# Performance work log

Hardware: AMD Instinct MI355X
Metric: run time of the kernel (lower is better)

## Reference

```python
import jax, jax.numpy as jnp
import numpy as np

B, L, D = 8, 30, 512
NS, NI = 21, 8  # n_slot_caps = n_slots+1, n_intent_caps = n_intents+1


def setup_inputs() -> dict:
    key = jax.random.key(0)
    ks = jax.random.split(key, 6)
    s = 0.02  # keep pose magnitudes sane
    return {
        "token_features": jax.random.normal(ks[0], (B, L, D), jnp.float32),
        "cls_token": jax.random.normal(ks[1], (B, D), jnp.float32),
        "w_route_ws": jax.random.normal(ks[2], (L, NS, D), jnp.float32) * s,
        "w_pose_ws": jax.random.normal(ks[3], (L, NS, D, D), jnp.float32) * s,
        "w_route_si": jax.random.normal(ks[4], (NS, NI, D), jnp.float32) * s,
        "w_pose_si": jax.random.normal(ks[5], (NS, NI, D, D), jnp.float32) * s,
    }


def reference(token_features, cls_token, w_route_ws, w_pose_ws, w_route_si, w_pose_si):
    d_model = token_features.shape[-1]
    # ---- route words -> slots ----
    a_words = token_features.sum(-1) / d_model                      # (b, l)
    c_ws = jax.nn.softmax(
        jnp.einsum('lnj,blj->bln', w_route_ws, token_features), axis=-1)  # (b, l, n_slot)
    wc = c_ws * a_words[:, :, None]                                 # (b, l, n_slot)
    weighted_c = wc.sum(axis=1)                                     # (b, n_slot)
    a_slots = weighted_c / a_words.sum(-1, keepdims=True)           # (b, n_slot)
    u_hat_slots = jnp.einsum('lnij,blj->blni', w_pose_ws, token_features)  # (b, l, n_slot, d)
    u_slots = jnp.einsum('bls,blsk->bsk', wc, u_hat_slots) / weighted_c[:, :, None]
    slots = jnp.argmax(c_ws, axis=-1)                               # (b, l)
    # ---- route slots -> intents ----
    c_si = jax.nn.softmax(
        jnp.einsum('sij,bsj->bsi', w_route_si, u_slots), axis=-1)   # (b, n_slot, n_int)
    wc2 = c_si * a_slots[:, :, None]                                # (b, n_slot, n_int)
    weighted_c2 = wc2.sum(axis=1)                                   # (b, n_int)
    a_intents = weighted_c2 / a_slots.sum(-1, keepdims=True)        # (b, n_int)
    u_hat_intents = jnp.einsum('sijk,bsk->bsik', w_pose_si, u_slots)  # (b, n_slot, n_int, d)
    u_intents = jnp.einsum('bsi,bsik->bik', wc2, u_hat_intents) / weighted_c2[:, :, None]
    # ---- argmax dispatch + cls residual ----
    max_idx = jnp.argmax(a_intents, axis=-1)                        # (b,)
    poses = jnp.take_along_axis(u_intents, max_idx[:, None, None], axis=1)[:, 0, :]
    intents = cls_token + poses                                     # (b, d)
    return (slots, intents)
```

## Files before the change

kernel.cpp:

```cpp
#include <hip/hip_runtime.h>

#define B 8
#define L 30
#define D 512
#define NS 21
#define NI 8
#define LC 5
#define LPC (L / LC)

__global__ void __launch_bounds__(256) k_phase_a(
    const float* __restrict__ x,
    const float* __restrict__ w_route_ws,
    float* __restrict__ wc,
    float* __restrict__ a_words,
    float* __restrict__ slots_out) {
  __shared__ float logits[NS];
  int bl   = blockIdx.x;
  int l    = bl % L;
  int wave = threadIdx.x >> 6;
  int lane = threadIdx.x & 63;

  const float4* xp = (const float4*)(x + (size_t)bl * D) + lane * 2;
  float4 x0 = xp[0], x1 = xp[1];

  float aw = 0.f;
  if (wave == 0) {
    float s = x0.x + x0.y + x0.z + x0.w + x1.x + x1.y + x1.z + x1.w;
    #pragma unroll
    for (int o = 32; o > 0; o >>= 1) s += __shfl_xor(s, o, 64);
    aw = s / (float)D;
    if (lane == 0) a_words[bl] = aw;
  }

  for (int n = wave; n < NS; n += 4) {
    const float4* wp = (const float4*)(w_route_ws + (size_t)(l * NS + n) * D) + lane * 2;
    float4 w0 = wp[0], w1 = wp[1];
    float q = w0.x * x0.x + w0.y * x0.y + w0.z * x0.z + w0.w * x0.w
            + w1.x * x1.x + w1.y * x1.y + w1.z * x1.z + w1.w * x1.w;
    #pragma unroll
    for (int o = 32; o > 0; o >>= 1) q += __shfl_xor(q, o, 64);
    if (lane == 0) logits[n] = q;
  }
  __syncthreads();

  if (threadIdx.x == 0) {
    float m = logits[0]; int am = 0;
    #pragma unroll
    for (int n = 1; n < NS; n++) if (logits[n] > m) { m = logits[n]; am = n; }
    float e[NS]; float se = 0.f;
    #pragma unroll
    for (int n = 0; n < NS; n++) { e[n] = __expf(logits[n] - m); se += e[n]; }
    float sc = aw / se;
    #pragma unroll
    for (int n = 0; n < NS; n++) wc[(size_t)bl * NS + n] = e[n] * sc;
    slots_out[bl] = (float)am;
  }
}

__global__ void k_stats1(const float* __restrict__ wc,
                         const float* __restrict__ a_words,
                         float* __restrict__ weighted_c,
                         float* __restrict__ a_slots) {
  __shared__ float aw_sum[B];
  int t = threadIdx.x;
  if (t < B) {
    float s = 0.f;
    for (int l = 0; l < L; l++) s += a_words[t * L + l];
    aw_sum[t] = s;
  }
  __syncthreads();
  if (t < B * NS) {
    int b = t / NS, n = t % NS;
    float s = 0.f;
    for (int l = 0; l < L; l++) s += wc[(size_t)(b * L + l) * NS + n];
    weighted_c[t] = s;
    a_slots[t] = s / aw_sum[b];
  }
}

__global__ void __launch_bounds__(256) k_u_slots(
    const float* __restrict__ x,
    const float* __restrict__ w_pose_ws,
    const float* __restrict__ wc,
    float* __restrict__ u_part) {
  __shared__ float lwc[B * L];
  int bid   = blockIdx.x;
  int n     = bid / (32 * LC);
  int rem   = bid % (32 * LC);
  int itile = rem / LC;
  int lc    = rem % LC;
  int wave  = threadIdx.x >> 6;
  int lane  = threadIdx.x & 63;
  int i0    = itile * 16 + wave * 4;

  if (threadIdx.x < B * L) lwc[threadIdx.x] = wc[(size_t)threadIdx.x * NS + n];
  __syncthreads();

  float acc[4][B];
  #pragma unroll
  for (int r = 0; r < 4; r++)
    #pragma unroll
    for (int b = 0; b < B; b++) acc[r][b] = 0.f;

  int l0 = lc * LPC;
  for (int l = l0; l < l0 + LPC; l++) {
    const float* wrow = w_pose_ws + ((size_t)(l * NS + n) * D + i0) * D;
    float4 w0[4], w1[4];
    #pragma unroll
    for (int r = 0; r < 4; r++) {
      const float4* wp = (const float4*)(wrow + (size_t)r * D) + lane * 2;
      w0[r] = wp[0]; w1[r] = wp[1];
    }
    #pragma unroll
    for (int b = 0; b < B; b++) {
      const float4* xp = (const float4*)(x + (size_t)(b * L + l) * D) + lane * 2;
      float4 x0 = xp[0], x1 = xp[1];
      float wcl = lwc[b * L + l];
      #pragma unroll
      for (int r = 0; r < 4; r++) {
        float t = w0[r].x * x0.x + w0[r].y * x0.y + w0[r].z * x0.z + w0[r].w * x0.w
                + w1[r].x * x1.x + w1[r].y * x1.y + w1[r].z * x1.z + w1[r].w * x1.w;
        acc[r][b] += wcl * t;
      }
    }
  }
  #pragma unroll
  for (int r = 0; r < 4; r++)
    #pragma unroll
    for (int b = 0; b < B; b++)
      #pragma unroll
      for (int o = 32; o > 0; o >>= 1) acc[r][b] += __shfl_xor(acc[r][b], o, 64);
  if (lane == 0) {
    #pragma unroll
    for (int r = 0; r < 4; r++)
      #pragma unroll
      for (int b = 0; b < B; b++)
        u_part[(((size_t)lc * B + b) * NS + n) * D + (i0 + r)] = acc[r][b];
  }
}

__global__ void k_div_u(const float* __restrict__ u_part,
                        const float* __restrict__ weighted_c,
                        float* __restrict__ u_slots) {
  int bn = blockIdx.x;
  int b  = bn / NS, n = bn % NS;
  float wcn = weighted_c[bn];
  for (int k = threadIdx.x; k < D; k += 256) {
    float s = 0.f;
    #pragma unroll
    for (int lc = 0; lc < LC; lc++)
      s += u_part[(((size_t)lc * B + b) * NS + n) * D + k];
    u_slots[(size_t)bn * D + k] = s / wcn;
  }
}

__global__ void __launch_bounds__(256) k_route_si(
    const float* __restrict__ u_slots,
    const float* __restrict__ w_route_si,
    const float* __restrict__ a_slots,
    float* __restrict__ wc2) {
  __shared__ float logits[NI];
  int bs   = blockIdx.x;
  int s    = bs % NS;
  int wave = threadIdx.x >> 6;
  int lane = threadIdx.x & 63;

  const float4* up = (const float4*)(u_slots + (size_t)bs * D) + lane * 2;
  float4 u0 = up[0], u1 = up[1];

  for (int i = wave; i < NI; i += 4) {
    const float4* wp = (const float4*)(w_route_si + (size_t)(s * NI + i) * D) + lane * 2;
    float4 w0 = wp[0], w1 = wp[1];
    float q = w0.x * u0.x + w0.y * u0.y + w0.z * u0.z + w0.w * u0.w
            + w1.x * u1.x + w1.y * u1.y + w1.z * u1.z + w1.w * u1.w;
    #pragma unroll
    for (int o = 32; o > 0; o >>= 1) q += __shfl_xor(q, o, 64);
    if (lane == 0) logits[i] = q;
  }
  __syncthreads();
  if (threadIdx.x == 0) {
    float m = logits[0];
    #pragma unroll
    for (int i = 1; i < NI; i++) m = fmaxf(m, logits[i]);
    float e[NI]; float se = 0.f;
    #pragma unroll
    for (int i = 0; i < NI; i++) { e[i] = __expf(logits[i] - m); se += e[i]; }
    float sc = a_slots[bs] / se;
    #pragma unroll
    for (int i = 0; i < NI; i++) wc2[(size_t)bs * NI + i] = e[i] * sc;
  }
}

__global__ void k_stats2(const float* __restrict__ wc2,
                         const float* __restrict__ a_slots,
                         float* __restrict__ weighted_c2,
                         int* __restrict__ max_idx) {
  __shared__ float asum[B];
  __shared__ float ai[B * NI];
  int t = threadIdx.x;
  if (t < B) {
    float s = 0.f;
    for (int n = 0; n < NS; n++) s += a_slots[t * NS + n];
    asum[t] = s;
  }
  float w = 0.f;
  if (t < B * NI) {
    int b = t / NI, i = t % NI;
    for (int ss = 0; ss < NS; ss++) w += wc2[(size_t)(b * NS + ss) * NI + i];
    weighted_c2[t] = w;
  }
  __syncthreads();
  if (t < B * NI) ai[t] = w / asum[t / NI];
  __syncthreads();
  if (t < B) {
    float m = ai[t * NI]; int am = 0;
    #pragma unroll
    for (int i = 1; i < NI; i++) { float v = ai[t * NI + i]; if (v > m) { m = v; am = i; } }
    max_idx[t] = am;
  }
}

__global__ void __launch_bounds__(256) k_colsum(
    const float* __restrict__ w_pose_si,
    const int* __restrict__ max_idx,
    float* __restrict__ colsum_part) {
  int blk = blockIdx.x;
  int si  = blk >> 2;
  int i   = si & (NI - 1);
  int jc  = blk & 3;
  bool sel = false;
  #pragma unroll
  for (int b = 0; b < B; b++) sel |= (max_idx[b] == i);
  if (!sel) return;

  int t  = threadIdx.x;
  int k4 = t & 127;
  int jg = t >> 7;
  const float4* wb = (const float4*)(w_pose_si + (size_t)si * D * D) + k4;
  int j0 = jc * 128 + jg * 64;
  float4 s = {0.f, 0.f, 0.f, 0.f};
  #pragma unroll 4
  for (int j = j0; j < j0 + 64; j++) {
    float4 v = wb[(size_t)j * (D / 4)];
    s.x += v.x; s.y += v.y; s.z += v.z; s.w += v.w;
  }
  __shared__ float4 part[128];
  if (jg == 0) part[k4] = s;
  __syncthreads();
  if (jg == 1) {
    float4 p = part[k4];
    p.x += s.x; p.y += s.y; p.z += s.z; p.w += s.w;
    ((float4*)colsum_part)[(size_t)(jc * NS * NI + si) * (D / 4) + k4] = p;
  }
}

__global__ void k_final2(const float* __restrict__ cls,
                         const float* __restrict__ u_slots,
                         const float* __restrict__ wc2,
                         const float* __restrict__ weighted_c2,
                         const int* __restrict__ max_idx,
                         const float* __restrict__ colsum_part,
                         float* __restrict__ out_intents) {
  int b = blockIdx.x, k = threadIdx.x;
  int i = max_idx[b];
  float acc = 0.f;
  for (int s = 0; s < NS; s++) {
    float cs = 0.f;
    #pragma unroll
    for (int jc = 0; jc < 4; jc++)
      cs += colsum_part[(size_t)(jc * NS * NI + s * NI + i) * D + k];
    acc += wc2[(size_t)(b * NS + s) * NI + i] *
           u_slots[(size_t)(b * NS + s) * D + k] * cs;
  }
  out_intents[b * D + k] = cls[b * D + k] + acc / weighted_c2[b * NI + i];
}

extern "C" void kernel_launch(void* const* d_in, const int* in_sizes, int n_in,
                              void* d_out, int out_size, void* d_ws, size_t ws_size,
                              hipStream_t stream) {
  const float* x    = (const float*)d_in[0];
  const float* cls  = (const float*)d_in[1];
  const float* wrws = (const float*)d_in[2];
  const float* wpws = (const float*)d_in[3];
  const float* wrsi = (const float*)d_in[4];
  const float* wpsi = (const float*)d_in[5];

  float* out         = (float*)d_out;
  float* slots_out   = out;
  float* intents_out = out + B * L;

  float* wsf         = (float*)d_ws;
  float* wc          = wsf;
  float* a_words     = wc + B * L * NS;
  float* weighted_c  = a_words + B * L;
  float* a_slots     = weighted_c + B * NS;
  float* u_slots     = a_slots + B * NS;
  float* u_part      = u_slots + B * NS * D;
  float* wc2         = u_part + LC * B * NS * D;
  float* weighted_c2 = wc2 + B * NS * NI;
  int*   max_idx     = (int*)(weighted_c2 + B * NI);
  float* colsum_part = (float*)(max_idx + 8);

  k_phase_a<<<B * L, 256, 0, stream>>>(x, wrws, wc, a_words, slots_out);
  k_stats1<<<1, 256, 0, stream>>>(wc, a_words, weighted_c, a_slots);
  k_u_slots<<<NS * 32 * LC, 256, 0, stream>>>(x, wpws, wc, u_part);
  k_div_u<<<B * NS, 256, 0, stream>>>(u_part, weighted_c, u_slots);
  k_route_si<<<B * NS, 256, 0, stream>>>(u_slots, wrsi, a_slots, wc2);
  k_stats2<<<1, 256, 0, stream>>>(wc2, a_slots, weighted_c2, max_idx);
  k_colsum<<<NS * NI * 4, 256, 0, stream>>>(wpsi, max_idx, colsum_part);
  k_final2<<<B, 512, 0, stream>>>(cls, u_slots, wc2, weighted_c2, max_idx,
                                  colsum_part, intents_out);
}
```

Measured before the change: 1.003 ms.

## Fold slot stats into div kernel, coalesce float4 loads, split L into six chunks

Removes the single-block k_stats1 launch by computing weighted_c and a_slots inside k_div_u with a wave reduction per (b, slot) block. Float4 loads change from two adjacent vectors per lane to a lane-strided pattern (lane and lane+64), so each wave instruction reads a contiguous span. The L split for the big pose GEMV goes from 5 to 6 chunks, giving more blocks and a larger partial buffer to reduce. The dominant cost is streaming the large w_pose_ws tensor, so the gains depend on bandwidth and on dropping one serial launch.

```diff
diff --git a/kernel.cpp b/kernel.cpp
--- a/kernel.cpp
+++ b/kernel.cpp
@@ -5,7 +5,7 @@
 #define D 512
 #define NS 21
 #define NI 8
-#define LC 5
+#define LC 6
 #define LPC (L / LC)
 
 __global__ void __launch_bounds__(256) k_phase_a(
@@ -20,8 +20,8 @@
   int wave = threadIdx.x >> 6;
   int lane = threadIdx.x & 63;
 
-  const float4* xp = (const float4*)(x + (size_t)bl * D) + lane * 2;
-  float4 x0 = xp[0], x1 = xp[1];
+  const float4* xp = (const float4*)(x + (size_t)bl * D);
+  float4 x0 = xp[lane], x1 = xp[lane + 64];
 
   float aw = 0.f;
   if (wave == 0) {
@@ -33,8 +33,8 @@
   }
 
   for (int n = wave; n < NS; n += 4) {
-    const float4* wp = (const float4*)(w_route_ws + (size_t)(l * NS + n) * D) + lane * 2;
-    float4 w0 = wp[0], w1 = wp[1];
+    const float4* wp = (const float4*)(w_route_ws + (size_t)(l * NS + n) * D);
+    float4 w0 = wp[lane], w1 = wp[lane + 64];
     float q = w0.x * x0.x + w0.y * x0.y + w0.z * x0.z + w0.w * x0.w
             + w1.x * x1.x + w1.y * x1.y + w1.z * x1.z + w1.w * x1.w;
     #pragma unroll
@@ -54,27 +54,6 @@
     #pragma unroll
     for (int n = 0; n < NS; n++) wc[(size_t)bl * NS + n] = e[n] * sc;
     slots_out[bl] = (float)am;
-  }
-}
-
-__global__ void k_stats1(const float* __restrict__ wc,
-                         const float* __restrict__ a_words,
-                         float* __restrict__ weighted_c,
-                         float* __restrict__ a_slots) {
-  __shared__ float aw_sum[B];
-  int t = threadIdx.x;
-  if (t < B) {
-    float s = 0.f;
-    for (int l = 0; l < L; l++) s += a_words[t * L + l];
-    aw_sum[t] = s;
-  }
-  __syncthreads();
-  if (t < B * NS) {
-    int b = t / NS, n = t % NS;
-    float s = 0.f;
-    for (int l = 0; l < L; l++) s += wc[(size_t)(b * L + l) * NS + n];
-    weighted_c[t] = s;
-    a_slots[t] = s / aw_sum[b];
   }
 }
 
@@ -108,13 +87,13 @@
     float4 w0[4], w1[4];
     #pragma unroll
     for (int r = 0; r < 4; r++) {
-      const float4* wp = (const float4*)(wrow + (size_t)r * D) + lane * 2;
-      w0[r] = wp[0]; w1[r] = wp[1];
+      const float4* wp = (const float4*)(wrow + (size_t)r * D);
+      w0[r] = wp[lane]; w1[r] = wp[lane + 64];
     }
     #pragma unroll
     for (int b = 0; b < B; b++) {
-      const float4* xp = (const float4*)(x + (size_t)(b * L + l) * D) + lane * 2;
-      float4 x0 = xp[0], x1 = xp[1];
+      const float4* xp = (const float4*)(x + (size_t)(b * L + l) * D);
+      float4 x0 = xp[lane], x1 = xp[lane + 64];
       float wcl = lwc[b * L + l];
       #pragma unroll
       for (int r = 0; r < 4; r++) {
@@ -139,18 +118,37 @@
   }
 }
 
-__global__ void k_div_u(const float* __restrict__ u_part,
-                        const float* __restrict__ weighted_c,
-                        float* __restrict__ u_slots) {
+__global__ void __launch_bounds__(256) k_div_u(
+    const float* __restrict__ u_part,
+    const float* __restrict__ wc,
+    const float* __restrict__ a_words,
+    float* __restrict__ a_slots,
+    float* __restrict__ u_slots) {
+  __shared__ float s_wcn;
   int bn = blockIdx.x;
   int b  = bn / NS, n = bn % NS;
-  float wcn = weighted_c[bn];
-  for (int k = threadIdx.x; k < D; k += 256) {
+  int t  = threadIdx.x;
+  if (t < 64) {
+    float sw = 0.f, sa = 0.f;
+    if (t < L) {
+      sw = wc[(size_t)(b * L + t) * NS + n];
+      sa = a_words[b * L + t];
+    }
+    #pragma unroll
+    for (int o = 32; o > 0; o >>= 1) {
+      sw += __shfl_xor(sw, o, 64);
+      sa += __shfl_xor(sa, o, 64);
+    }
+    if (t == 0) { s_wcn = sw; a_slots[bn] = sw / sa; }
+  }
+  __syncthreads();
+  float inv = 1.f / s_wcn;
+  for (int k = t; k < D; k += 256) {
     float s = 0.f;
     #pragma unroll
     for (int lc = 0; lc < LC; lc++)
       s += u_part[(((size_t)lc * B + b) * NS + n) * D + k];
-    u_slots[(size_t)bn * D + k] = s / wcn;
+    u_slots[(size_t)bn * D + k] = s * inv;
   }
 }
 
@@ -165,12 +163,12 @@
   int wave = threadIdx.x >> 6;
   int lane = threadIdx.x & 63;
 
-  const float4* up = (const float4*)(u_slots + (size_t)bs * D) + lane * 2;
-  float4 u0 = up[0], u1 = up[1];
+  const float4* up = (const float4*)(u_slots + (size_t)bs * D);
+  float4 u0 = up[lane], u1 = up[lane + 64];
 
   for (int i = wave; i < NI; i += 4) {
-    const float4* wp = (const float4*)(w_route_si + (size_t)(s * NI + i) * D) + lane * 2;
-    float4 w0 = wp[0], w1 = wp[1];
+    const float4* wp = (const float4*)(w_route_si + (size_t)(s * NI + i) * D);
+    float4 w0 = wp[lane], w1 = wp[lane + 64];
     float q = w0.x * u0.x + w0.y * u0.y + w0.z * u0.z + w0.w * u0.w
             + w1.x * u1.x + w1.y * u1.y + w1.z * u1.z + w1.w * u1.w;
     #pragma unroll
@@ -292,8 +290,7 @@
   float* wsf         = (float*)d_ws;
   float* wc          = wsf;
   float* a_words     = wc + B * L * NS;
-  float* weighted_c  = a_words + B * L;
-  float* a_slots     = weighted_c + B * NS;
+  float* a_slots     = a_words + B * L;
   float* u_slots     = a_slots + B * NS;
   float* u_part      = u_slots + B * NS * D;
   float* wc2         = u_part + LC * B * NS * D;
@@ -302,9 +299,8 @@
   float* colsum_part = (float*)(max_idx + 8);
 
   k_phase_a<<<B * L, 256, 0, stream>>>(x, wrws, wc, a_words, slots_out);
-  k_stats1<<<1, 256, 0, stream>>>(wc, a_words, weighted_c, a_slots);
   k_u_slots<<<NS * 32 * LC, 256, 0, stream>>>(x, wpws, wc, u_part);
-  k_div_u<<<B * NS, 256, 0, stream>>>(u_part, weighted_c, u_slots);
+  k_div_u<<<B * NS, 256, 0, stream>>>(u_part, wc, a_words, a_slots, u_slots);
   k_route_si<<<B * NS, 256, 0, stream>>>(u_slots, wrsi, a_slots, wc2);
   k_stats2<<<1, 256, 0, stream>>>(wc2, a_slots, weighted_c2, max_idx);
   k_colsum<<<NS * NI * 4, 256, 0, stream>>>(wpsi, max_idx, colsum_part);
```

Result: faster. 953.7 us (-5.0%).
